# Optimization experiments

Hardware: AMD Instinct MI355X
Metric: run time of the kernel (lower is better)

Reference implementation:

```python
import jax, jax.numpy as jnp
import numpy as np

D_MODEL = 2048
N_HEADS = 16
N_KV_HEADS = 4
HEAD_DIM = D_MODEL // N_HEADS  # 128
ROPE_THETA = 1000000.0


def _quant_rowwise(x):
    """Symmetric int8 rowwise quantization over the last dim (simulated in f32)."""
    s = jnp.max(jnp.abs(x), axis=-1, keepdims=True) / 127.0
    s = jnp.maximum(s, 1e-8)
    q = jnp.clip(jnp.round(x / s), -127.0, 127.0)
    return q, s


def _rope_tables(seq_len, head_dim, theta, dtype):
    inv_freq = 1.0 / (theta ** (jnp.arange(0, head_dim, 2, dtype=jnp.float32) / head_dim))
    pos = jnp.arange(seq_len, dtype=jnp.float32)
    freqs = pos[:, None] * inv_freq[None, :]            # (T, hd/2)
    emb = jnp.concatenate([freqs, freqs], axis=-1)      # (T, hd)
    return jnp.cos(emb).astype(dtype), jnp.sin(emb).astype(dtype)


def _rotate_half(x):
    h = x.shape[-1] // 2
    return jnp.concatenate([-x[..., h:], x[..., :h]], axis=-1)


def setup_inputs() -> dict:
    key = jax.random.key(0)
    k0, k1, k2, k3, k4 = jax.random.split(key, 5)
    x = jax.random.normal(k0, (1, 2048, D_MODEL), dtype=jnp.float32)
    sc = D_MODEL ** -0.5
    wq = jax.random.normal(k1, (N_HEADS * HEAD_DIM, D_MODEL), dtype=jnp.float32) * sc
    wk = jax.random.normal(k2, (N_KV_HEADS * HEAD_DIM, D_MODEL), dtype=jnp.float32) * sc
    wv = jax.random.normal(k3, (N_KV_HEADS * HEAD_DIM, D_MODEL), dtype=jnp.float32) * sc
    wo = jax.random.normal(k4, (D_MODEL, N_HEADS * HEAD_DIM), dtype=jnp.float32) * sc
    return {"x": x, "wq": wq, "wk": wk, "wv": wv, "wo": wo}


def _int8_linear(qx, x_scale, w):
    # Per-output-channel int8 weight quant, int8 matmul, rowwise dequant.
    qw, w_scale = _quant_rowwise(w)                      # (O,D), (O,1)
    y = jnp.einsum('btd,od->bto', qx, qw)
    return y * x_scale * w_scale[:, 0][None, None, :]


def reference(x, wq, wk, wv, wo):
    B, T, D = x.shape
    H, Hkv, hd = N_HEADS, N_KV_HEADS, HEAD_DIM
    scale = hd ** -0.5

    # Shared int8-quantized input for QKV projections
    qx, x_scale = _quant_rowwise(x)                      # (B,T,D), (B,T,1)
    q = _int8_linear(qx, x_scale, wq).reshape(B, T, H, hd).transpose(0, 2, 1, 3)
    k = _int8_linear(qx, x_scale, wk).reshape(B, T, Hkv, hd).transpose(0, 2, 1, 3)
    v = _int8_linear(qx, x_scale, wv).reshape(B, T, Hkv, hd).transpose(0, 2, 1, 3)

    # RoPE
    cos, sin = _rope_tables(T, hd, ROPE_THETA, x.dtype)  # (T, hd)
    q = q * cos + _rotate_half(q) * sin
    k = k * cos + _rotate_half(k) * sin

    # GQA: repeat kv heads
    rep = H // Hkv
    k = jnp.repeat(k, rep, axis=1)
    v = jnp.repeat(v, rep, axis=1)

    # int8 attention core: rowwise quantize q,k,v, int8 score matmul, dequant
    qq, qs = _quant_rowwise(q)
    kq, ks = _quant_rowwise(k)
    vq, vs = _quant_rowwise(v)
    scores = jnp.einsum('bhqd,bhkd->bhqk', qq, kq) * qs * jnp.swapaxes(ks, -1, -2) * scale
    causal = jnp.tril(jnp.ones((T, T), dtype=bool))
    scores = jnp.where(causal[None, None], scores, jnp.finfo(scores.dtype).min)
    attn = jax.nn.softmax(scores, axis=-1)
    out = jnp.einsum('bhqk,bhkd->bhqd', attn, vq * vs)   # dequant v inside matmul

    out = out.transpose(0, 2, 1, 3).reshape(B, T, H * hd)
    return out @ wo.T
```

## Files before the change

### kernel.cpp

```cpp
#include <hip/hip_runtime.h>
#include <cstdint>
#include <math.h>

#define TT 2048
#define DD 2048
#define NH 16
#define NKV 4
#define HD 128
#define SCALE_F 0.08838834764831845f
#define LOG2E 1.4426950408889634f

#if __has_builtin(__builtin_amdgcn_exp2f)
#define EXP2(x) __builtin_amdgcn_exp2f(x)
#else
#define EXP2(x) exp2f(x)
#endif

typedef int   i32x4 __attribute__((ext_vector_type(4)));
typedef float f32x4 __attribute__((ext_vector_type(4)));
typedef short s16x8 __attribute__((ext_vector_type(8)));

__device__ __forceinline__ i32x4 mfma_i8(i32x4 a, i32x4 b, i32x4 c) {
  return __builtin_amdgcn_mfma_i32_16x16x64_i8(a, b, c, 0, 0, 0);
}
__device__ __forceinline__ f32x4 mfma_bf16(s16x8 a, s16x8 b, f32x4 c) {
  return __builtin_amdgcn_mfma_f32_16x16x32_bf16(a, b, c, 0, 0, 0);
}
__device__ __forceinline__ uint32_t fbits(float f) {
  union { float f; uint32_t u; } x; x.f = f; return x.u;
}
__device__ __forceinline__ ushort bf16_rne(float v) {
  uint32_t u = fbits(v);
  return (ushort)((u + 0x7fffu + ((u >> 16) & 1u)) >> 16);
}
__device__ __forceinline__ float bf16_to_f(ushort h) {
  union { uint32_t u; float f; } x; x.u = ((uint32_t)h) << 16; return x.f;
}

__global__ __launch_bounds__(256)
void rope_table_kernel(float2* __restrict__ tab) {
  int idx = blockIdx.x * 256 + threadIdx.x;
  int t = idx >> 6, d = idx & 63;
  float inv = 1.0f / powf(1000000.0f, (float)d * (1.0f/64.0f));
  float ang = (float)t * inv;
  float sn, cs;
  sincosf(ang, &sn, &cs);
  tab[idx] = make_float2(cs, sn);
}

__global__ __launch_bounds__(256)
void quant_rows_kernel(const float* __restrict__ x, const float* __restrict__ wq,
                       const float* __restrict__ wk, const float* __restrict__ wv,
                       int8_t* __restrict__ qx, float* __restrict__ xs,
                       int8_t* __restrict__ qwq, float* __restrict__ wqs,
                       int8_t* __restrict__ qwk, float* __restrict__ wks,
                       int8_t* __restrict__ qwv, float* __restrict__ wvs) {
  int r = blockIdx.x;
  const float* src; int8_t* dst; float* sc; int row;
  if (r < 2048)      { src = x;  dst = qx;  sc = xs;  row = r; }
  else if (r < 4096) { src = wq; dst = qwq; sc = wqs; row = r - 2048; }
  else if (r < 4608) { src = wk; dst = qwk; sc = wks; row = r - 4096; }
  else               { src = wv; dst = qwv; sc = wvs; row = r - 4608; }
  src += (size_t)row * DD; dst += (size_t)row * DD;
  int tid = threadIdx.x;
  float4 v0 = ((const float4*)src)[2*tid];
  float4 v1 = ((const float4*)src)[2*tid+1];
  float m = fmaxf(fmaxf(fmaxf(fabsf(v0.x), fabsf(v0.y)), fmaxf(fabsf(v0.z), fabsf(v0.w))),
                  fmaxf(fmaxf(fabsf(v1.x), fabsf(v1.y)), fmaxf(fabsf(v1.z), fabsf(v1.w))));
  #pragma unroll
  for (int off = 1; off < 64; off <<= 1) m = fmaxf(m, __shfl_xor(m, off));
  __shared__ float wmax[4];
  if ((tid & 63) == 0) wmax[tid >> 6] = m;
  __syncthreads();
  m = fmaxf(fmaxf(wmax[0], wmax[1]), fmaxf(wmax[2], wmax[3]));
  float s = fmaxf(m / 127.0f, 1e-8f);
  if (tid == 0) sc[row] = s;
  float vv[8] = {v0.x, v0.y, v0.z, v0.w, v1.x, v1.y, v1.z, v1.w};
  uint32_t p0 = 0, p1 = 0;
  #pragma unroll
  for (int i = 0; i < 4; ++i) {
    int q = (int)fminf(fmaxf(rintf(vv[i] / s), -127.0f), 127.0f);
    p0 |= ((uint32_t)q & 0xffu) << (8*i);
  }
  #pragma unroll
  for (int i = 0; i < 4; ++i) {
    int q = (int)fminf(fmaxf(rintf(vv[4+i] / s), -127.0f), 127.0f);
    p1 |= ((uint32_t)q & 0xffu) << (8*i);
  }
  ((uint2*)dst)[tid] = make_uint2(p0, p1);
}

__global__ __launch_bounds__(128)
void proj_kernel(const int8_t* __restrict__ qx, const float* __restrict__ xs,
                 const int8_t* __restrict__ qwq, const float* __restrict__ wqs,
                 const int8_t* __restrict__ qwk, const float* __restrict__ wks,
                 const int8_t* __restrict__ qwv, const float* __restrict__ wvs,
                 const float2* __restrict__ ropet,
                 int8_t* __restrict__ qq, float* __restrict__ qsc_out,
                 int8_t* __restrict__ kq, float* __restrict__ ksc_out,
                 int8_t* __restrict__ vq, float* __restrict__ vsc_out) {
  int id  = blockIdx.x;
  int xcd = id & 7;
  int j   = id >> 3;
  int hg  = xcd >> 1;
  int th  = xcd & 1;
  int gh  = hg*6 + (j % 6);
  int tb  = th*16 + (j / 6);
  int t0  = tb * 64;

  const int8_t* wgt; const float* wsc; int8_t* outq; float* outs; bool doRope;
  if (gh < NH) {
    wgt = qwq + (size_t)gh*HD*DD; wsc = wqs + gh*HD;
    outq = qq + (size_t)gh*TT*HD; outs = qsc_out + (size_t)gh*TT; doRope = true;
  } else if (gh < NH + NKV) {
    int hh = gh - NH;
    wgt = qwk + (size_t)hh*HD*DD; wsc = wks + hh*HD;
    outq = kq + (size_t)hh*TT*HD; outs = ksc_out + (size_t)hh*TT; doRope = true;
  } else {
    int hh = gh - NH - NKV;
    wgt = qwv + (size_t)hh*HD*DD; wsc = wvs + hh*HD;
    outq = vq + (size_t)hh*TT*HD; outs = vsc_out + (size_t)hh*TT; doRope = false;
  }

  __shared__ int8_t As[64 * 144];
  __shared__ int8_t Bs[128 * 144];
  int tid = threadIdx.x;
  int w  = tid >> 6;
  int l  = tid & 63;
  int lg = l & 15;
  int lh = l >> 4;

  i32x4 acc[2][8];
  #pragma unroll
  for (int ti = 0; ti < 2; ++ti)
    #pragma unroll
    for (int tj = 0; tj < 8; ++tj) acc[ti][tj] = (i32x4){0,0,0,0};

  i32x4 prefA[4], prefB[8];

#define PROJ_ISSUE(KT)                                                          \
  {                                                                             \
    int kk0 = (KT) * 128;                                                       \
    _Pragma("unroll")                                                           \
    for (int i = 0; i < 4; ++i) {                                               \
      int idx = tid + i*128, r = idx >> 3, c = idx & 7;                         \
      prefA[i] = *(const i32x4*)&qx[(size_t)(t0 + r)*DD + kk0 + c*16];          \
    }                                                                           \
    _Pragma("unroll")                                                           \
    for (int i = 0; i < 8; ++i) {                                               \
      int idx = tid + i*128, r = idx >> 3, c = idx & 7;                         \
      prefB[i] = *(const i32x4*)&wgt[(size_t)r*DD + kk0 + c*16];                \
    }                                                                           \
  }

  PROJ_ISSUE(0);

  for (int kt = 0; kt < DD/128; ++kt) {
    __syncthreads();
    #pragma unroll
    for (int i = 0; i < 4; ++i) {
      int idx = tid + i*128, r = idx >> 3, c = idx & 7;
      *(i32x4*)&As[r*144 + c*16] = prefA[i];
    }
    #pragma unroll
    for (int i = 0; i < 8; ++i) {
      int idx = tid + i*128, r = idx >> 3, c = idx & 7;
      *(i32x4*)&Bs[r*144 + c*16] = prefB[i];
    }
    __syncthreads();
    if (kt + 1 < DD/128) PROJ_ISSUE(kt + 1);

    #pragma unroll
    for (int s = 0; s < 2; ++s) {
      i32x4 a0 = *(const i32x4*)&As[(w*32 + lg)*144      + s*64 + lh*16];
      i32x4 a1 = *(const i32x4*)&As[(w*32 + 16 + lg)*144 + s*64 + lh*16];
      #pragma unroll
      for (int tj = 0; tj < 8; ++tj) {
        i32x4 b = *(const i32x4*)&Bs[(tj*16 + lg)*144 + s*64 + lh*16];
        acc[0][tj] = mfma_i8(a0, b, acc[0][tj]);
        acc[1][tj] = mfma_i8(a1, b, acc[1][tj]);
      }
    }
  }
#undef PROJ_ISSUE

  float y[2][8][4];
  #pragma unroll
  for (int ti = 0; ti < 2; ++ti)
    #pragma unroll
    for (int rr = 0; rr < 4; ++rr) {
      int tl = w*32 + ti*16 + lh*4 + rr;
      float xsi = xs[t0 + tl];
      #pragma unroll
      for (int tj = 0; tj < 8; ++tj)
        y[ti][tj][rr] = (float)acc[ti][tj][rr] * xsi * wsc[tj*16 + lg];
    }

  if (doRope) {
    #pragma unroll
    for (int ti = 0; ti < 2; ++ti)
      #pragma unroll
      for (int rr = 0; rr < 4; ++rr) {
        int trow = t0 + w*32 + ti*16 + lh*4 + rr;
        const float2* tr = &ropet[trow * 64];
        #pragma unroll
        for (int tj = 0; tj < 4; ++tj) {
          float2 cssn = tr[tj*16 + lg];
          float lo = y[ti][tj][rr], hi = y[ti][tj+4][rr];
          y[ti][tj][rr]   = lo*cssn.x - hi*cssn.y;
          y[ti][tj+4][rr] = hi*cssn.x + lo*cssn.y;
        }
      }
  }

  __syncthreads();
  #pragma unroll
  for (int ti = 0; ti < 2; ++ti)
    #pragma unroll
    for (int rr = 0; rr < 4; ++rr) {
      int tl = w*32 + ti*16 + lh*4 + rr;
      float mx = fabsf(y[ti][0][rr]);
      #pragma unroll
      for (int tj = 1; tj < 8; ++tj) mx = fmaxf(mx, fabsf(y[ti][tj][rr]));
      mx = fmaxf(mx, __shfl_xor(mx, 1));
      mx = fmaxf(mx, __shfl_xor(mx, 2));
      mx = fmaxf(mx, __shfl_xor(mx, 4));
      mx = fmaxf(mx, __shfl_xor(mx, 8));
      float s = fmaxf(mx / 127.0f, 1e-8f);
      if (lg == 0) outs[t0 + tl] = s;
      #pragma unroll
      for (int tj = 0; tj < 8; ++tj) {
        int qv = (int)fminf(fmaxf(rintf(y[ti][tj][rr] / s), -127.0f), 127.0f);
        As[tl*144 + tj*16 + lg] = (int8_t)qv;
      }
    }
  __syncthreads();
  #pragma unroll
  for (int i = 0; i < 4; ++i) {
    int idx = tid + i*128, r = idx >> 3, c = idx & 7;
    *(i32x4*)&outq[(size_t)(t0 + r)*HD + c*16] = *(const i32x4*)&As[r*144 + c*16];
  }
}

__global__ __launch_bounds__(512)
void attn_mfma_kernel(const int8_t* __restrict__ qq, const float* __restrict__ qsc_in,
                      const int8_t* __restrict__ kq, const float* __restrict__ ksc_in,
                      const int8_t* __restrict__ vq, const float* __restrict__ vsc_in,
                      ushort* __restrict__ aoh, ushort* __restrict__ aol,
                      float* __restrict__ opA, float* __restrict__ opB,
                      float* __restrict__ ml) {
  int id = blockIdx.x;
  int h   = id / 30;
  int loc = id % 30;
  int qb2, c;
  if (loc < 12)      { qb2 = 15 - loc/3;        c = loc % 3; }
  else if (loc < 24) { qb2 = 11 - (loc - 12)/2; c = (loc - 12) % 2; }
  else               { qb2 = 5 - (loc - 24);    c = 0; }
  int nkt = 2*qb2 + 2;
  int nc  = (qb2 <= 5) ? 1 : ((qb2 <= 11) ? 2 : 3);
  int ktb = (c * nkt) / nc;
  int kte = ((c + 1) * nkt) / nc;
  int hk  = h >> 2;
  int qb0 = qb2 * 128;

  __shared__ int8_t Ks[64 * 144];
  __shared__ ushort Vt[128 * 72];
  __shared__ float  Pf[8][16 * 68];

  int tid = threadIdx.x;
  int w  = tid >> 6;
  int l  = tid & 63;
  int lg = l & 15;
  int lh = l >> 4;

  const int8_t* qp = &qq[((size_t)h*TT + qb0 + 16*w + lg)*HD + lh*16];
  i32x4 qa0 = *(const i32x4*)qp;
  i32x4 qa1 = *(const i32x4*)(qp + 64);

  int myq = qb0 + 16*w + lg;
  float qsl = qsc_in[(size_t)h*TT + myq] * (SCALE_F * LOG2E);

  float mrun = -1e30f, lrun = 0.f;
  f32x4 acc_o[8];
  #pragma unroll
  for (int dt = 0; dt < 8; ++dt) acc_o[dt] = (f32x4){0.f, 0.f, 0.f, 0.f};

  int sr = tid >> 3, scc = tid & 7;
  int m2 = tid & 31, d0 = (tid >> 5) * 8;

  i32x4 kreg;
  int2  vreg0, vreg1;

#define ISSUE_LOADS(KT)                                                         \
  {                                                                             \
    int kk0 = (KT) * 64;                                                        \
    kreg = *(const i32x4*)&kq[((size_t)hk*TT + kk0 + sr)*HD + scc*16];          \
    const int8_t* vp = &vq[((size_t)hk*TT + kk0 + 2*m2)*HD + d0];               \
    vreg0 = *(const int2*)vp;                                                   \
    vreg1 = *(const int2*)(vp + HD);                                            \
  }

  ISSUE_LOADS(ktb);

  for (int kt = ktb; kt < kte; ++kt) {
    int k0 = kt * 64;
    __syncthreads();
    *(i32x4*)&Ks[sr*144 + scc*16] = kreg;
    #pragma unroll
    for (int jj = 0; jj < 4; ++jj) {
      int a0 = (vreg0.x << (24 - 8*jj)) >> 24;
      int b0 = (vreg1.x << (24 - 8*jj)) >> 24;
      *(uint32_t*)&Vt[(d0 + jj)*72 + 2*m2] =
          (fbits((float)a0) >> 16) | ((fbits((float)b0) >> 16) << 16);
      int a1 = (vreg0.y << (24 - 8*jj)) >> 24;
      int b1 = (vreg1.y << (24 - 8*jj)) >> 24;
      *(uint32_t*)&Vt[(d0 + 4 + jj)*72 + 2*m2] =
          (fbits((float)a1) >> 16) | ((fbits((float)b1) >> 16) << 16);
    }
    __syncthreads();
    if (kt + 1 < kte) ISSUE_LOADS(kt + 1);

    i32x4 sacc[4];
    #pragma unroll
    for (int t = 0; t < 4; ++t) sacc[t] = (i32x4){0, 0, 0, 0};
    __builtin_amdgcn_s_setprio(1);
    #pragma unroll
    for (int t = 0; t < 4; ++t) {
      const int8_t* kp = &Ks[(16*t + lg)*144 + lh*16];
      i32x4 b0 = *(const i32x4*)kp;
      i32x4 b1 = *(const i32x4*)(kp + 64);
      sacc[t] = mfma_i8(b0, qa0, sacc[t]);
      sacc[t] = mfma_i8(b1, qa1, sacc[t]);
    }
    __builtin_amdgcn_s_setprio(0);

    f32x4 ksv4[4], vsv4[4];
    #pragma unroll
    for (int t = 0; t < 4; ++t) {
      ksv4[t] = *(const f32x4*)&ksc_in[(size_t)hk*TT + k0 + 16*t + 4*lh];
      vsv4[t] = *(const f32x4*)&vsc_in[(size_t)hk*TT + k0 + 16*t + 4*lh];
    }

    bool maskTile = (kt >= nkt - 2);
    float sf[4][4];
    #pragma unroll
    for (int t = 0; t < 4; ++t)
      #pragma unroll
      for (int rr = 0; rr < 4; ++rr) {
        float v = (float)sacc[t][rr] * qsl * ksv4[t][rr];
        if (maskTile) {
          int kkg = k0 + 16*t + 4*lh + rr;
          v = (kkg <= myq) ? v : -1e30f;
        }
        sf[t][rr] = v;
      }

    float rm = sf[0][0];
    #pragma unroll
    for (int t = 0; t < 4; ++t)
      #pragma unroll
      for (int rr = 0; rr < 4; ++rr) rm = fmaxf(rm, sf[t][rr]);
    rm = fmaxf(rm, __shfl_xor(rm, 16));
    rm = fmaxf(rm, __shfl_xor(rm, 32));
    float mnew = fmaxf(mrun, rm);
    float corr = EXP2(mrun - mnew);
    mrun = mnew;
    float p[4][4];
    float ps = 0.f;
    #pragma unroll
    for (int t = 0; t < 4; ++t)
      #pragma unroll
      for (int rr = 0; rr < 4; ++rr) { p[t][rr] = EXP2(sf[t][rr] - mnew); ps += p[t][rr]; }
    ps += __shfl_xor(ps, 16);
    ps += __shfl_xor(ps, 32);
    lrun = lrun * corr + ps;

    #pragma unroll
    for (int t = 0; t < 4; ++t) {
      f32x4 pw;
      #pragma unroll
      for (int rr = 0; rr < 4; ++rr) pw[rr] = p[t][rr] * vsv4[t][rr];
      *(f32x4*)&Pf[w][lg*68 + 16*t + 4*lh] = pw;
    }

    #pragma unroll
    for (int dt = 0; dt < 8; ++dt)
      #pragma unroll
      for (int rr = 0; rr < 4; ++rr) acc_o[dt][rr] *= corr;

    s16x8 pahi[2], palo[2];
    #pragma unroll
    for (int kb = 0; kb < 2; ++kb) {
      const float* pr = &Pf[w][lg*68 + kb*32 + lh*8];
      f32x4 x0 = *(const f32x4*)pr;
      f32x4 x1 = *(const f32x4*)(pr + 4);
      float xv[8] = {x0.x, x0.y, x0.z, x0.w, x1.x, x1.y, x1.z, x1.w};
      float lv[8];
      #pragma unroll
      for (int jv = 0; jv < 8; ++jv) {
        uint32_t hb = fbits(xv[jv]) & 0xffff0000u;
        union { uint32_t u; float f; } hf; hf.u = hb;
        lv[jv] = xv[jv] - hf.f;
      }
      union { uint32_t u[4]; s16x8 v; } H, L;
      #pragma unroll
      for (int jj = 0; jj < 4; ++jj) {
        H.u[jj] = (fbits(xv[2*jj]) >> 16) | (fbits(xv[2*jj+1]) & 0xffff0000u);
        L.u[jj] = (fbits(lv[2*jj]) >> 16) | (fbits(lv[2*jj+1]) & 0xffff0000u);
      }
      pahi[kb] = H.v; palo[kb] = L.v;
    }

    __builtin_amdgcn_s_setprio(1);
    #pragma unroll
    for (int dt = 0; dt < 8; ++dt) {
      #pragma unroll
      for (int kb = 0; kb < 2; ++kb) {
        s16x8 vb = *(const s16x8*)&Vt[(16*dt + lg)*72 + kb*32 + lh*8];
        acc_o[dt] = mfma_bf16(vb, pahi[kb], acc_o[dt]);
        acc_o[dt] = mfma_bf16(vb, palo[kb], acc_o[dt]);
      }
    }
    __builtin_amdgcn_s_setprio(0);
  }
#undef ISSUE_LOADS

  if (nc == 1) {
    float invv = 1.0f / lrun;
    size_t base = (size_t)myq*DD + (size_t)h*HD;
    #pragma unroll
    for (int dt = 0; dt < 8; ++dt) {
      ushort4 Hv, Lv;
      float v0 = acc_o[dt][0]*invv, v1 = acc_o[dt][1]*invv;
      float v2 = acc_o[dt][2]*invv, v3 = acc_o[dt][3]*invv;
      Hv.x = bf16_rne(v0); Hv.y = bf16_rne(v1); Hv.z = bf16_rne(v2); Hv.w = bf16_rne(v3);
      Lv.x = bf16_rne(v0 - bf16_to_f(Hv.x)); Lv.y = bf16_rne(v1 - bf16_to_f(Hv.y));
      Lv.z = bf16_rne(v2 - bf16_to_f(Hv.z)); Lv.w = bf16_rne(v3 - bf16_to_f(Hv.w));
      *(ushort4*)&aoh[base + 16*dt + 4*lh] = Hv;
      *(ushort4*)&aol[base + 16*dt + 4*lh] = Lv;
    }
  } else {
    int base = (qb2 <= 11) ? (qb2 - 6)*2 : 12 + (qb2 - 12)*3;
    int slot = h*24 + base + c;
    float* op = (slot < 160) ? (opA + (size_t)slot * 16384)
                             : (opB + (size_t)(slot - 160) * 16384);
    op += (size_t)(16*w + lg) * 128;
    #pragma unroll
    for (int dt = 0; dt < 8; ++dt)
      *(f32x4*)&op[16*dt + 4*lh] = acc_o[dt];
    if (lh == 0) {
      ml[slot*256 + 16*w + lg]       = mrun;
      ml[slot*256 + 128 + 16*w + lg] = lrun;
    }
  }
}

__global__ __launch_bounds__(256)
void merge_kernel(const float* __restrict__ opA, const float* __restrict__ opB,
                  const float* __restrict__ ml,
                  ushort* __restrict__ aoh, ushort* __restrict__ aol) {
  int tile = blockIdx.x;
  int h = tile / 10;
  int qb2 = 6 + tile % 10;
  int nc = (qb2 <= 11) ? 2 : 3;
  int sbase = h*24 + ((qb2 <= 11) ? (qb2 - 6)*2 : 12 + (qb2 - 12)*3);

  int tid = threadIdx.x;
  int row = tid >> 1;
  int cseg = (tid & 1) * 64;

  float mv[3], lv[3];
  const float* pp[3];
  #pragma unroll
  for (int i = 0; i < 3; ++i) {
    int slot = sbase + ((i < nc) ? i : 0);
    const float* p = (slot < 160) ? (opA + (size_t)slot * 16384)
                                  : (opB + (size_t)(slot - 160) * 16384);
    pp[i] = p + (size_t)row * 128 + cseg;
    if (i < nc) {
      mv[i] = ml[slot*256 + row];
      lv[i] = ml[slot*256 + 128 + row];
    } else {
      mv[i] = -1e30f;
      lv[i] = 0.f;
    }
  }
  float M = fmaxf(fmaxf(mv[0], mv[1]), mv[2]);
  float wgt[3];
  float L = 0.f;
  #pragma unroll
  for (int i = 0; i < 3; ++i) { wgt[i] = EXP2(mv[i] - M); L += wgt[i]*lv[i]; }
  float inv = 1.0f / L;

  size_t ob = (size_t)(qb2*128 + row)*DD + (size_t)h*HD + cseg;
  #pragma unroll
  for (int c4 = 0; c4 < 16; ++c4) {
    f32x4 a0 = *(const f32x4*)&pp[0][c4*4];
    f32x4 a1 = *(const f32x4*)&pp[1][c4*4];
    f32x4 a2 = *(const f32x4*)&pp[2][c4*4];
    ushort4 Hv, Lv;
    #pragma unroll
    for (int e = 0; e < 4; ++e) {
      float v = (wgt[0]*a0[e] + wgt[1]*a1[e] + wgt[2]*a2[e]) * inv;
      ushort hb = bf16_rne(v);
      ushort lb = bf16_rne(v - bf16_to_f(hb));
      ((ushort*)&Hv)[e] = hb;
      ((ushort*)&Lv)[e] = lb;
    }
    *(ushort4*)&aoh[ob + c4*4] = Hv;
    *(ushort4*)&aol[ob + c4*4] = Lv;
  }
}

__global__ __launch_bounds__(256)
void wcvt_kernel(const float* __restrict__ wom, ushort* __restrict__ woh,
                 ushort* __restrict__ wol) {
  size_t base = ((size_t)blockIdx.x * 256 + threadIdx.x) * 8;
  float4 a = *(const float4*)&wom[base];
  float4 b = *(const float4*)&wom[base + 4];
  float vv[8] = {a.x, a.y, a.z, a.w, b.x, b.y, b.z, b.w};
  s16x8 H, L;
  #pragma unroll
  for (int j = 0; j < 8; ++j) {
    ushort hb = bf16_rne(vv[j]);
    float lo = vv[j] - bf16_to_f(hb);
    H[j] = (short)hb;
    L[j] = (short)bf16_rne(lo);
  }
  *(s16x8*)&woh[base] = H;
  *(s16x8*)&wol[base] = L;
}

__global__ __launch_bounds__(256)
void wo_gemm_kernel(const ushort* __restrict__ aoh, const ushort* __restrict__ aol,
                    const ushort* __restrict__ woh, const ushort* __restrict__ wol,
                    float* __restrict__ outp) {
  int id  = blockIdx.x;
  int xcd = id & 7;
  int j   = id >> 3;
  int tb  = xcd*4 + (j >> 4);
  int ob  = j & 15;
  int t0  = tb * 64;
  int o0  = ob * 128;

  __shared__ ushort AH[64 * 72];
  __shared__ ushort AL[64 * 72];
  __shared__ ushort BH[128 * 72];
  __shared__ ushort BL[128 * 72];
  int tid = threadIdx.x;
  int wv4 = tid >> 6;
  int wr = wv4 >> 1, wc = wv4 & 1;
  int l  = tid & 63;
  int lg = l & 15;
  int lh = l >> 4;

  f32x4 acc[2][4];
  #pragma unroll
  for (int ti = 0; ti < 2; ++ti)
    #pragma unroll
    for (int tj = 0; tj < 4; ++tj) acc[ti][tj] = (f32x4){0.f,0.f,0.f,0.f};

  s16x8 pAH[2], pAL[2], pBH[4], pBL[4];

#define WO_ISSUE(KT)                                                            \
  {                                                                             \
    int k0 = (KT) * 64;                                                         \
    _Pragma("unroll")                                                           \
    for (int i = 0; i < 2; ++i) {                                               \
      int idx = tid + i*256, r = idx >> 3, c = idx & 7;                         \
      size_t ga = (size_t)(t0 + r)*DD + k0 + c*8;                               \
      pAH[i] = *(const s16x8*)&aoh[ga];                                         \
      pAL[i] = *(const s16x8*)&aol[ga];                                         \
    }                                                                           \
    _Pragma("unroll")                                                           \
    for (int i = 0; i < 4; ++i) {                                               \
      int idx = tid + i*256, r = idx >> 3, c = idx & 7;                         \
      size_t gb = (size_t)(o0 + r)*DD + k0 + c*8;                               \
      pBH[i] = *(const s16x8*)&woh[gb];                                         \
      pBL[i] = *(const s16x8*)&wol[gb];                                         \
    }                                                                           \
  }

  WO_ISSUE(0);

  for (int kt = 0; kt < DD/64; ++kt) {
    __syncthreads();
    #pragma unroll
    for (int i = 0; i < 2; ++i) {
      int idx = tid + i*256, r = idx >> 3, c = idx & 7;
      *(s16x8*)&AH[r*72 + c*8] = pAH[i];
      *(s16x8*)&AL[r*72 + c*8] = pAL[i];
    }
    #pragma unroll
    for (int i = 0; i < 4; ++i) {
      int idx = tid + i*256, r = idx >> 3, c = idx & 7;
      *(s16x8*)&BH[r*72 + c*8] = pBH[i];
      *(s16x8*)&BL[r*72 + c*8] = pBL[i];
    }
    __syncthreads();
    if (kt + 1 < DD/64) WO_ISSUE(kt + 1);

    #pragma unroll
    for (int s = 0; s < 2; ++s) {
      s16x8 ah[2], al[2];
      #pragma unroll
      for (int ti = 0; ti < 2; ++ti) {
        int ab = (wr*32 + ti*16 + lg)*72 + s*32 + lh*8;
        ah[ti] = *(const s16x8*)&AH[ab];
        al[ti] = *(const s16x8*)&AL[ab];
      }
      #pragma unroll
      for (int tj = 0; tj < 4; ++tj) {
        int bb = (wc*64 + tj*16 + lg)*72 + s*32 + lh*8;
        s16x8 bh = *(const s16x8*)&BH[bb];
        s16x8 bl = *(const s16x8*)&BL[bb];
        #pragma unroll
        for (int ti = 0; ti < 2; ++ti) {
          acc[ti][tj] = mfma_bf16(ah[ti], bh, acc[ti][tj]);
          acc[ti][tj] = mfma_bf16(ah[ti], bl, acc[ti][tj]);
          acc[ti][tj] = mfma_bf16(al[ti], bh, acc[ti][tj]);
        }
      }
    }
  }
#undef WO_ISSUE

  #pragma unroll
  for (int ti = 0; ti < 2; ++ti)
    #pragma unroll
    for (int tj = 0; tj < 4; ++tj)
      #pragma unroll
      for (int rr = 0; rr < 4; ++rr) {
        int t = t0 + wr*32 + ti*16 + lh*4 + rr;
        int o = o0 + wc*64 + tj*16 + lg;
        outp[(size_t)t*DD + o] = acc[ti][tj][rr];
      }
}

extern "C" void kernel_launch(void* const* d_in, const int* in_sizes, int n_in,
                              void* d_out, int out_size, void* d_ws, size_t ws_size,
                              hipStream_t stream) {
  (void)in_sizes; (void)n_in; (void)out_size; (void)ws_size;
  const float* x  = (const float*)d_in[0];
  const float* wq = (const float*)d_in[1];
  const float* wk = (const float*)d_in[2];
  const float* wv = (const float*)d_in[3];
  const float* wo = (const float*)d_in[4];
  float* out = (float*)d_out;

  char* ws = (char*)d_ws;
  const size_t MB = 1048576;
  int8_t* qx  = (int8_t*)(ws);
  int8_t* qwq = (int8_t*)(ws + 4*MB);
  int8_t* qwk = (int8_t*)(ws + 8*MB);
  int8_t* qwv = (int8_t*)(ws + 9*MB);
  int8_t* qqp = (int8_t*)(ws + 10*MB);
  int8_t* kqp = (int8_t*)(ws + 14*MB);
  int8_t* vqp = (int8_t*)(ws + 15*MB);
  float* xs  = (float*)(ws + 16*MB);
  float* wqs = xs + 2048;
  float* wks = wqs + 2048;
  float* wvs = wks + 512;
  float* qsc = wvs + 512;
  float* ksc = qsc + (size_t)NH*TT;
  float* vsc = ksc + (size_t)NKV*TT;
  ushort* aoh = (ushort*)(ws + 16*MB + 262144);
  ushort* aol = (ushort*)(ws + 24*MB + 262144);
  float2* ropet = (float2*)(ws + 16*MB + 262144);
  float* opA = (float*)(ws);
  float* opB = out;
  float* mlb = (float*)((char*)out + 15*MB + 524288);
  ushort* woh = (ushort*)(ws);
  ushort* wol = (ushort*)(ws + 8*MB);

  rope_table_kernel<<<512, 256, 0, stream>>>(ropet);
  quant_rows_kernel<<<5120, 256, 0, stream>>>(x, wq, wk, wv,
                                              qx, xs, qwq, wqs, qwk, wks, qwv, wvs);
  proj_kernel<<<768, 128, 0, stream>>>(
      qx, xs, qwq, wqs, qwk, wks, qwv, wvs, ropet,
      qqp, qsc, kqp, ksc, vqp, vsc);
  attn_mfma_kernel<<<480, 512, 0, stream>>>(
      qqp, qsc, kqp, ksc, vqp, vsc, aoh, aol, opA, opB, mlb);
  merge_kernel<<<160, 256, 0, stream>>>(opA, opB, mlb, aoh, aol);
  wcvt_kernel<<<2048, 256, 0, stream>>>(wo, woh, wol);
  wo_gemm_kernel<<<512, 256, 0, stream>>>(aoh, aol, woh, wol, out);
}
```

Measured before the change: 178.2 us.

## Replace split-bf16 output projection with two-level int8 split GEMM

The final output projection stops using bf16 hi/lo operand pairs and instead quantizes both activations and weights rowwise into two int8 planes (hi and residual lo at scale 128). It then runs three int8 MFMA products into integer accumulators and dequantizes with per-row scales in the epilogue. The aim is to halve operand bytes and use the denser int8 MFMA path, and setprio is added around the MFMA block. In exchange it adds a separate activation quantization pass and changes numerics to an approximately 14-bit fixed-point representation, which may cost accuracy.

Result: faster. 167.6 us (-5.9%).

```diff
diff --git a/kernel.cpp b/kernel.cpp
--- a/kernel.cpp
+++ b/kernel.cpp
@@ -513,27 +513,81 @@
 }
 
 __global__ __launch_bounds__(256)
-void wcvt_kernel(const float* __restrict__ wom, ushort* __restrict__ woh,
-                 ushort* __restrict__ wol) {
-  size_t base = ((size_t)blockIdx.x * 256 + threadIdx.x) * 8;
-  float4 a = *(const float4*)&wom[base];
-  float4 b = *(const float4*)&wom[base + 4];
-  float vv[8] = {a.x, a.y, a.z, a.w, b.x, b.y, b.z, b.w};
-  s16x8 H, L;
+void aquant_kernel(const ushort* __restrict__ aoh, const ushort* __restrict__ aol,
+                   int8_t* __restrict__ ahi, int8_t* __restrict__ alo,
+                   float* __restrict__ sa) {
+  int r = blockIdx.x;
+  int tid = threadIdx.x;
+  s16x8 hv = *(const s16x8*)&aoh[(size_t)r*DD + tid*8];
+  s16x8 lvv = *(const s16x8*)&aol[(size_t)r*DD + tid*8];
+  float v[8];
+  #pragma unroll
+  for (int j = 0; j < 8; ++j)
+    v[j] = bf16_to_f((ushort)hv[j]) + bf16_to_f((ushort)lvv[j]);
+  float m = fabsf(v[0]);
+  #pragma unroll
+  for (int j = 1; j < 8; ++j) m = fmaxf(m, fabsf(v[j]));
+  #pragma unroll
+  for (int off = 1; off < 64; off <<= 1) m = fmaxf(m, __shfl_xor(m, off));
+  __shared__ float wmax[4];
+  if ((tid & 63) == 0) wmax[tid >> 6] = m;
+  __syncthreads();
+  m = fmaxf(fmaxf(wmax[0], wmax[1]), fmaxf(wmax[2], wmax[3]));
+  float s = fmaxf(m * (1.0f/16256.0f), 1e-30f);
+  if (tid == 0) sa[r] = s;
+  float inv = 1.0f / s;
+  uint32_t h0 = 0, h1 = 0, l0 = 0, l1 = 0;
   #pragma unroll
   for (int j = 0; j < 8; ++j) {
-    ushort hb = bf16_rne(vv[j]);
-    float lo = vv[j] - bf16_to_f(hb);
-    H[j] = (short)hb;
-    L[j] = (short)bf16_rne(lo);
-  }
-  *(s16x8*)&woh[base] = H;
-  *(s16x8*)&wol[base] = L;
+    float q = v[j] * inv;
+    int hi = (int)fminf(fmaxf(rintf(q * (1.0f/128.0f)), -127.0f), 127.0f);
+    int lo = (int)fminf(fmaxf(rintf(q - 128.0f*(float)hi), -127.0f), 127.0f);
+    if (j < 4) { h0 |= ((uint32_t)hi & 0xffu) << (8*j);     l0 |= ((uint32_t)lo & 0xffu) << (8*j); }
+    else       { h1 |= ((uint32_t)hi & 0xffu) << (8*(j-4)); l1 |= ((uint32_t)lo & 0xffu) << (8*(j-4)); }
+  }
+  ((uint2*)&ahi[(size_t)r*DD])[tid] = make_uint2(h0, h1);
+  ((uint2*)&alo[(size_t)r*DD])[tid] = make_uint2(l0, l1);
 }
 
 __global__ __launch_bounds__(256)
-void wo_gemm_kernel(const ushort* __restrict__ aoh, const ushort* __restrict__ aol,
-                    const ushort* __restrict__ woh, const ushort* __restrict__ wol,
+void wquant_kernel(const float* __restrict__ wom,
+                   int8_t* __restrict__ bhi, int8_t* __restrict__ blo,
+                   float* __restrict__ sb) {
+  int r = blockIdx.x;
+  int tid = threadIdx.x;
+  const float* src = wom + (size_t)r*DD + tid*8;
+  float4 a = *(const float4*)src;
+  float4 b = *(const float4*)(src + 4);
+  float v[8] = {a.x, a.y, a.z, a.w, b.x, b.y, b.z, b.w};
+  float m = fabsf(v[0]);
+  #pragma unroll
+  for (int j = 1; j < 8; ++j) m = fmaxf(m, fabsf(v[j]));
+  #pragma unroll
+  for (int off = 1; off < 64; off <<= 1) m = fmaxf(m, __shfl_xor(m, off));
+  __shared__ float wmax[4];
+  if ((tid & 63) == 0) wmax[tid >> 6] = m;
+  __syncthreads();
+  m = fmaxf(fmaxf(wmax[0], wmax[1]), fmaxf(wmax[2], wmax[3]));
+  float s = fmaxf(m * (1.0f/16256.0f), 1e-30f);
+  if (tid == 0) sb[r] = s;
+  float inv = 1.0f / s;
+  uint32_t h0 = 0, h1 = 0, l0 = 0, l1 = 0;
+  #pragma unroll
+  for (int j = 0; j < 8; ++j) {
+    float q = v[j] * inv;
+    int hi = (int)fminf(fmaxf(rintf(q * (1.0f/128.0f)), -127.0f), 127.0f);
+    int lo = (int)fminf(fmaxf(rintf(q - 128.0f*(float)hi), -127.0f), 127.0f);
+    if (j < 4) { h0 |= ((uint32_t)hi & 0xffu) << (8*j);     l0 |= ((uint32_t)lo & 0xffu) << (8*j); }
+    else       { h1 |= ((uint32_t)hi & 0xffu) << (8*(j-4)); l1 |= ((uint32_t)lo & 0xffu) << (8*(j-4)); }
+  }
+  ((uint2*)&bhi[(size_t)r*DD])[tid] = make_uint2(h0, h1);
+  ((uint2*)&blo[(size_t)r*DD])[tid] = make_uint2(l0, l1);
+}
+
+__global__ __launch_bounds__(256)
+void wo_gemm_kernel(const int8_t* __restrict__ ahi, const int8_t* __restrict__ alo,
+                    const int8_t* __restrict__ bhi, const int8_t* __restrict__ blo,
+                    const float* __restrict__ sa, const float* __restrict__ sb,
                     float* __restrict__ outp) {
   int id  = blockIdx.x;
   int xcd = id & 7;
@@ -543,10 +597,10 @@
   int t0  = tb * 64;
   int o0  = ob * 128;
 
-  __shared__ ushort AH[64 * 72];
-  __shared__ ushort AL[64 * 72];
-  __shared__ ushort BH[128 * 72];
-  __shared__ ushort BL[128 * 72];
+  __shared__ int8_t AH[64 * 72];
+  __shared__ int8_t AL[64 * 72];
+  __shared__ int8_t BH[128 * 72];
+  __shared__ int8_t BL[128 * 72];
   int tid = threadIdx.x;
   int wv4 = tid >> 6;
   int wr = wv4 >> 1, wc = wv4 & 1;
@@ -554,30 +608,30 @@
   int lg = l & 15;
   int lh = l >> 4;
 
-  f32x4 acc[2][4];
+  i32x4 acc_h[2][4], acc_m[2][4];
   #pragma unroll
   for (int ti = 0; ti < 2; ++ti)
     #pragma unroll
-    for (int tj = 0; tj < 4; ++tj) acc[ti][tj] = (f32x4){0.f,0.f,0.f,0.f};
-
-  s16x8 pAH[2], pAL[2], pBH[4], pBL[4];
+    for (int tj = 0; tj < 4; ++tj) {
+      acc_h[ti][tj] = (i32x4){0,0,0,0};
+      acc_m[ti][tj] = (i32x4){0,0,0,0};
+    }
+
+  i32x4 pAH, pAL, pBH[2], pBL[2];
+  int ar = tid >> 2, ac = tid & 3;
 
 #define WO_ISSUE(KT)                                                            \
   {                                                                             \
     int k0 = (KT) * 64;                                                         \
+    size_t ga = (size_t)(t0 + ar)*DD + k0 + ac*16;                              \
+    pAH = *(const i32x4*)&ahi[ga];                                              \
+    pAL = *(const i32x4*)&alo[ga];                                              \
     _Pragma("unroll")                                                           \
     for (int i = 0; i < 2; ++i) {                                               \
-      int idx = tid + i*256, r = idx >> 3, c = idx & 7;                         \
-      size_t ga = (size_t)(t0 + r)*DD + k0 + c*8;                               \
-      pAH[i] = *(const s16x8*)&aoh[ga];                                         \
-      pAL[i] = *(const s16x8*)&aol[ga];                                         \
-    }                                                                           \
-    _Pragma("unroll")                                                           \
-    for (int i = 0; i < 4; ++i) {                                               \
-      int idx = tid + i*256, r = idx >> 3, c = idx & 7;                         \
-      size_t gb = (size_t)(o0 + r)*DD + k0 + c*8;                               \
-      pBH[i] = *(const s16x8*)&woh[gb];                                         \
-      pBL[i] = *(const s16x8*)&wol[gb];                                         \
+      int idx = tid + i*256, r = idx >> 2, c = idx & 3;                         \
+      size_t gb = (size_t)(o0 + r)*DD + k0 + c*16;                              \
+      pBH[i] = *(const i32x4*)&bhi[gb];                                         \
+      pBL[i] = *(const i32x4*)&blo[gb];                                         \
     }                                                                           \
   }
 
@@ -585,56 +639,60 @@
 
   for (int kt = 0; kt < DD/64; ++kt) {
     __syncthreads();
+    *(i32x4*)&AH[ar*72 + ac*16] = pAH;
+    *(i32x4*)&AL[ar*72 + ac*16] = pAL;
     #pragma unroll
     for (int i = 0; i < 2; ++i) {
-      int idx = tid + i*256, r = idx >> 3, c = idx & 7;
-      *(s16x8*)&AH[r*72 + c*8] = pAH[i];
-      *(s16x8*)&AL[r*72 + c*8] = pAL[i];
-    }
-    #pragma unroll
-    for (int i = 0; i < 4; ++i) {
-      int idx = tid + i*256, r = idx >> 3, c = idx & 7;
-      *(s16x8*)&BH[r*72 + c*8] = pBH[i];
-      *(s16x8*)&BL[r*72 + c*8] = pBL[i];
+      int idx = tid + i*256, r = idx >> 2, c = idx & 3;
+      *(i32x4*)&BH[r*72 + c*16] = pBH[i];
+      *(i32x4*)&BL[r*72 + c*16] = pBL[i];
     }
     __syncthreads();
     if (kt + 1 < DD/64) WO_ISSUE(kt + 1);
 
-    #pragma unroll
-    for (int s = 0; s < 2; ++s) {
-      s16x8 ah[2], al[2];
+    i32x4 a_h[2], a_l[2];
+    #pragma unroll
+    for (int ti = 0; ti < 2; ++ti) {
+      int ab = (wr*32 + ti*16 + lg)*72 + lh*16;
+      a_h[ti] = *(const i32x4*)&AH[ab];
+      a_l[ti] = *(const i32x4*)&AL[ab];
+    }
+    __builtin_amdgcn_s_setprio(1);
+    #pragma unroll
+    for (int tj = 0; tj < 4; ++tj) {
+      int bb = (wc*64 + tj*16 + lg)*72 + lh*16;
+      i32x4 b_h = *(const i32x4*)&BH[bb];
+      i32x4 b_l = *(const i32x4*)&BL[bb];
       #pragma unroll
       for (int ti = 0; ti < 2; ++ti) {
-        int ab = (wr*32 + ti*16 + lg)*72 + s*32 + lh*8;
-        ah[ti] = *(const s16x8*)&AH[ab];
-        al[ti] = *(const s16x8*)&AL[ab];
-      }
-      #pragma unroll
-      for (int tj = 0; tj < 4; ++tj) {
-        int bb = (wc*64 + tj*16 + lg)*72 + s*32 + lh*8;
-        s16x8 bh = *(const s16x8*)&BH[bb];
-        s16x8 bl = *(const s16x8*)&BL[bb];
-        #pragma unroll
-        for (int ti = 0; ti < 2; ++ti) {
-          acc[ti][tj] = mfma_bf16(ah[ti], bh, acc[ti][tj]);
-          acc[ti][tj] = mfma_bf16(ah[ti], bl, acc[ti][tj]);
-          acc[ti][tj] = mfma_bf16(al[ti], bh, acc[ti][tj]);
-        }
-      }
-    }
+        acc_h[ti][tj] = mfma_i8(a_h[ti], b_h, acc_h[ti][tj]);
+        acc_m[ti][tj] = mfma_i8(a_h[ti], b_l, acc_m[ti][tj]);
+        acc_m[ti][tj] = mfma_i8(a_l[ti], b_h, acc_m[ti][tj]);
+      }
+    }
+    __builtin_amdgcn_s_setprio(0);
   }
 #undef WO_ISSUE
 
   #pragma unroll
-  for (int ti = 0; ti < 2; ++ti)
-    #pragma unroll
-    for (int tj = 0; tj < 4; ++tj)
+  for (int ti = 0; ti < 2; ++ti) {
+    float sav[4];
+    #pragma unroll
+    for (int rr = 0; rr < 4; ++rr)
+      sav[rr] = sa[t0 + wr*32 + ti*16 + lh*4 + rr];
+    #pragma unroll
+    for (int tj = 0; tj < 4; ++tj) {
+      int o = o0 + wc*64 + tj*16 + lg;
+      float sbo = sb[o];
       #pragma unroll
       for (int rr = 0; rr < 4; ++rr) {
         int t = t0 + wr*32 + ti*16 + lh*4 + rr;
-        int o = o0 + wc*64 + tj*16 + lg;
-        outp[(size_t)t*DD + o] = acc[ti][tj][rr];
-      }
+        float v = sav[rr] * sbo *
+                  (16384.0f * (float)acc_h[ti][tj][rr] + 128.0f * (float)acc_m[ti][tj][rr]);
+        outp[(size_t)t*DD + o] = v;
+      }
+    }
+  }
 }
 
 extern "C" void kernel_launch(void* const* d_in, const int* in_sizes, int n_in,
@@ -670,8 +728,12 @@
   float* opA = (float*)(ws);
   float* opB = out;
   float* mlb = (float*)((char*)out + 15*MB + 524288);
-  ushort* woh = (ushort*)(ws);
-  ushort* wol = (ushort*)(ws + 8*MB);
+  int8_t* ahi = (int8_t*)(ws);
+  int8_t* alo = (int8_t*)(ws + 4*MB);
+  int8_t* bhi = (int8_t*)(ws + 8*MB);
+  int8_t* blo = (int8_t*)(ws + 12*MB);
+  float* sa = (float*)(ws + 16*MB);
+  float* sb = sa + 2048;
 
   rope_table_kernel<<<512, 256, 0, stream>>>(ropet);
   quant_rows_kernel<<<5120, 256, 0, stream>>>(x, wq, wk, wv,
@@ -682,6 +744,7 @@
   attn_mfma_kernel<<<480, 512, 0, stream>>>(
       qqp, qsc, kqp, ksc, vqp, vsc, aoh, aol, opA, opB, mlb);
   merge_kernel<<<160, 256, 0, stream>>>(opA, opB, mlb, aoh, aol);
-  wcvt_kernel<<<2048, 256, 0, stream>>>(wo, woh, wol);
-  wo_gemm_kernel<<<512, 256, 0, stream>>>(aoh, aol, woh, wol, out);
-}
+  aquant_kernel<<<2048, 256, 0, stream>>>(aoh, aol, ahi, alo, sa);
+  wquant_kernel<<<2048, 256, 0, stream>>>(wo, bhi, blo, sb);
+  wo_gemm_kernel<<<512, 256, 0, stream>>>(ahi, alo, bhi, blo, sa, sb, out);
+}
```
